# Optimization experiments

Hardware: AMD Instinct MI355X
Metric: run time of the kernel (lower is better)

The kernel has to match this reference:

```python
import jax, jax.numpy as jnp
import numpy as np

MOE_TOP_K = 2
MOE_GATE_NORM_STD = 1.0  # moe_gate_norm_std


def setup_inputs() -> dict:
    key = jax.random.key(0)
    k1, k2, k3, k4 = jax.random.split(key, 4)
    T, D, E = 16384, 2048, 8
    return {
        "x": jax.random.normal(k1, (T, D), dtype=jnp.float32),
        "wg_weight": jax.random.normal(k2, (E, D), dtype=jnp.float32) * 0.02,
        "gate_map_weight": jax.random.normal(k3, (E, E), dtype=jnp.float32) * 0.1,
        "gate_residual": jax.random.normal(k4, (T, E), dtype=jnp.float32),
    }


def reference(x, wg_weight, gate_map_weight, gate_residual):
    # Router GEMM in fp32 (module force-casts wg and input to float32)
    logits = jnp.einsum("td,ed->te", x.astype(jnp.float32), wg_weight)  # [T, E]
    # gate_residual path: gate_map Linear(E, E, bias=False)
    logits = logits + jnp.einsum("te,fe->tf", gate_residual, gate_map_weight)

    num_experts = wg_weight.shape[0]
    # gating(): moe_use_mixtral_gating=False, moe_use_logits_norm=True
    # torch.std is unbiased (ddof=1)
    logits_std = jnp.std(logits, axis=1, keepdims=True, ddof=1)
    probs = jax.nn.softmax(logits / (logits_std / MOE_GATE_NORM_STD), axis=1)
    gates, indices = jax.lax.top_k(probs, MOE_TOP_K)  # [T, K]
    # zero out routing to the last expert, then renormalize
    gates = jnp.where(indices == num_experts - 1, jnp.zeros_like(gates), gates)
    gates = gates / jnp.sum(gates, axis=1, keepdims=True)
    # Dense equivalent of the per-expert nonzero-gather dict: (indices, gates)
    # fully determines expert_info[e] = (tokens where indices==e, matching gates).
    return gates, indices, logits
```

## Files before the change

kernel.cpp:

```cpp
#include <hip/hip_runtime.h>
#include <hip/hip_bf16.h>
#include <stdint.h>


#define DCONST 2048

typedef float f32x4 __attribute__((ext_vector_type(4)));

__device__ __forceinline__ unsigned long long shfl_xor_u64(unsigned long long v, int m) {
    int lo = __shfl_xor((int)(uint32_t)v, m, 64);
    int hi = __shfl_xor((int)(uint32_t)(v >> 32), m, 64);
    return ((unsigned long long)(uint32_t)hi << 32) | (unsigned long long)(uint32_t)lo;
}

__global__ __launch_bounds__(256, 2)
void router_gemm(const float* __restrict__ x,
                 const float* __restrict__ wg,
                 float* __restrict__ ws,
                 int T)
{
    const int wave = threadIdx.x >> 6;
    const int lane = threadIdx.x & 63;
    const int W    = blockIdx.x * 4 + wave;

    #pragma unroll 1
    for (int s = 0; s < 2; ++s) {
        const int id    = W + s * 2048;
        const int g     = id & 7;
        const int trow  = (id >> 3) * 32;
        const int tb0   = trow >> 3;

        const float* wgp = wg + g * 256 + (lane << 2);
        f32x4 w8[8];
        #pragma unroll
        for (int e = 0; e < 8; ++e)
            w8[e] = *(const f32x4*)(wgp + (size_t)e * DCONST);

        const float* xp = x + (size_t)trow * DCONST + g * 256 + (lane << 2);

        f32x4 A[8], B[8];

        #define LOADB(buf, b)                                                 \
            { _Pragma("unroll")                                               \
              for (int i = 0; i < 8; ++i)                                     \
                  buf[i] = __builtin_nontemporal_load(                        \
                      (const f32x4*)(xp + (size_t)((b) * 8 + i) * DCONST)); }

        #define DOBATCH(buf, b)                                               \
            { float acc[64];                                                  \
              _Pragma("unroll")                                               \
              for (int v = 0; v < 64; ++v) acc[v] = 0.f;                      \
              _Pragma("unroll")                                               \
              for (int i = 0; i < 8; ++i) {                                   \
                  _Pragma("unroll")                                           \
                  for (int e = 0; e < 8; ++e) {                               \
                      float a = acc[i * 8 + e];                               \
                      a += buf[i].x * w8[e].x;                                \
                      a += buf[i].y * w8[e].y;                                \
                      a += buf[i].z * w8[e].z;                                \
                      a += buf[i].w * w8[e].w;                                \
                      acc[i * 8 + e] = a;                                     \
                  }                                                           \
              }                                                               \
              _Pragma("unroll")                                               \
              for (int m = 1; m < 64; m <<= 1) {                              \
                  const bool up = (lane & m) != 0;                            \
                  _Pragma("unroll")                                           \
                  for (int v = 0; v < 64; v += 2 * m) {                       \
                      const float keep = up ? acc[v + m] : acc[v];            \
                      const float send = up ? acc[v] : acc[v + m];            \
                      const float got  = __shfl_xor(send, m, 64);             \
                      acc[v] = keep + got;                                    \
                  }                                                           \
              }                                                               \
              ws[(size_t)(tb0 + (b)) * 512 + g * 64 + lane] = acc[0]; }

        LOADB(A, 0);
        #pragma unroll 1
        for (int b = 0; b < 4; b += 2) {
            LOADB(B, b + 1);
            DOBATCH(A, b);
            if (b + 2 < 4) LOADB(A, b + 2);
            DOBATCH(B, b + 1);
        }
    }
}

__global__ __launch_bounds__(256)
void router_epilogue(const float* __restrict__ ws,
                     const float* __restrict__ gm,
                     const float* __restrict__ gr,
                     float* __restrict__ out,
                     int T)
{
    const int wave = threadIdx.x >> 6;
    const int lane = threadIdx.x & 63;
    const int tb   = blockIdx.x * 4 + wave;
    const int t0   = tb * 8;

    float logit = 0.f;
    #pragma unroll
    for (int g = 0; g < 8; ++g)
        logit += ws[(size_t)tb * 512 + g * 64 + lane];

    const int tt = lane >> 3;
    const int f  = lane & 7;
    const int t  = t0 + tt;

    const float4 ga = *(const float4*)(gr + (size_t)t * 8);
    const float4 gb = *(const float4*)(gr + (size_t)t * 8 + 4);
    const float4 ma = *(const float4*)(gm + f * 8);
    const float4 mb = *(const float4*)(gm + f * 8 + 4);
    logit += ga.x * ma.x + ga.y * ma.y + ga.z * ma.z + ga.w * ma.w
           + gb.x * mb.x + gb.y * mb.y + gb.z * mb.z + gb.w * mb.w;

    out[(size_t)4 * T + (size_t)t0 * 8 + lane] = logit;

    float s = logit;
    s += __shfl_xor(s, 1, 64);
    s += __shfl_xor(s, 2, 64);
    s += __shfl_xor(s, 4, 64);
    const float mean = s * 0.125f;
    float d2 = (logit - mean) * (logit - mean);
    d2 += __shfl_xor(d2, 1, 64);
    d2 += __shfl_xor(d2, 2, 64);
    d2 += __shfl_xor(d2, 4, 64);
    const float stdv = sqrtf(d2 / 7.0f);

    uint32_t ob = __float_as_uint(logit);
    ob = (ob & 0x80000000u) ? ~ob : (ob | 0x80000000u);
    unsigned long long k1 = ((unsigned long long)ob << 8) | (unsigned long long)(7 - f);
    unsigned long long k2 = 0ull;
    #pragma unroll
    for (int m = 1; m <= 4; m <<= 1) {
        const unsigned long long o1 = shfl_xor_u64(k1, m);
        const unsigned long long o2 = shfl_xor_u64(k2, m);
        const unsigned long long hi = k1 > o1 ? k1 : o1;
        const unsigned long long lo = k1 > o1 ? o1 : k1;
        const unsigned long long so = k2 > o2 ? k2 : o2;
        k1 = hi;
        k2 = lo > so ? lo : so;
    }
    const int i1 = 7 - (int)(k1 & 0xFFull);
    const int i2 = 7 - (int)(k2 & 0xFFull);
    uint32_t b1 = (uint32_t)(k1 >> 8), b2 = (uint32_t)(k2 >> 8);
    b1 = (b1 & 0x80000000u) ? (b1 ^ 0x80000000u) : ~b1;
    b2 = (b2 & 0x80000000u) ? (b2 ^ 0x80000000u) : ~b2;
    const float l1 = __uint_as_float(b1);
    const float l2 = __uint_as_float(b2);

    float g0, g1;
    if (i1 == 7)      { g0 = 0.f; g1 = 1.f; }
    else if (i2 == 7) { g0 = 1.f; g1 = 0.f; }
    else {
        const float p = 1.0f / (1.0f + __expf(-(l1 - l2) / stdv));
        g0 = p; g1 = 1.0f - p;
    }

    if (f == 0) out[(size_t)2 * t]             = g0;
    if (f == 1) out[(size_t)2 * t + 1]         = g1;
    if (f == 2) out[(size_t)2 * T + 2 * t]     = (float)i1;
    if (f == 3) out[(size_t)2 * T + 2 * t + 1] = (float)i2;
}

extern "C" void kernel_launch(void* const* d_in, const int* in_sizes, int n_in,
                              void* d_out, int out_size, void* d_ws, size_t ws_size,
                              hipStream_t stream) {
    const float* x  = (const float*)d_in[0];
    const float* wg = (const float*)d_in[1];
    const float* gm = (const float*)d_in[2];
    const float* gr = (const float*)d_in[3];
    float* ws = (float*)d_ws;
    const int T = in_sizes[0] / DCONST;

    router_gemm<<<512, 256, 0, stream>>>(x, wg, ws, T);

    const int epi_blocks = T / 32;
    router_epilogue<<<epi_blocks, 256, 0, stream>>>(ws, gm, gr, (float*)d_out, T);
}
```

Measured before the change: 190.0 us.

## Stream router GEMM activations via direct global-to-LDS loads with double buffering

The activation tiles now go straight from global memory into per-wave LDS double buffers through global_load_lds, with hand-placed vmcnt waits. Previously they were loaded into registers with nontemporal loads. Each batch is read back from LDS into registers just before the FMA and shuffle reduction. The expert weight loads are also hoisted out of the two-pass loop, since the group index is the same on both passes. The aim is to free registers and overlap memory traffic with compute, at the cost of 64KB of LDS per block and fragile raw waitcnt encodings.

```diff
diff --git a/kernel.cpp b/kernel.cpp
--- a/kernel.cpp
+++ b/kernel.cpp
@@ -6,6 +6,12 @@
 #define DCONST 2048
 
 typedef float f32x4 __attribute__((ext_vector_type(4)));
+
+__device__ __forceinline__ void gload_lds16(const float* g, float* l) {
+    __builtin_amdgcn_global_load_lds(
+        (const __attribute__((address_space(1))) void*)g,
+        (__attribute__((address_space(3))) void*)l, 16, 0, 0);
+}
 
 __device__ __forceinline__ unsigned long long shfl_xor_u64(unsigned long long v, int m) {
     int lo = __shfl_xor((int)(uint32_t)v, m, 64);
@@ -23,31 +29,37 @@
     const int lane = threadIdx.x & 63;
     const int W    = blockIdx.x * 4 + wave;
 
+    __shared__ float lds[4][2][DCONST];
+    float* buf0 = &lds[wave][0][0];
+    float* buf1 = &lds[wave][1][0];
+
+    const int g     = W & 7;
+    const int trow0 = (W >> 3) * 32;
+
+    const float* wgp = wg + g * 256 + (lane << 2);
+    f32x4 w8[8];
+    #pragma unroll
+    for (int e = 0; e < 8; ++e)
+        w8[e] = *(const f32x4*)(wgp + (size_t)e * DCONST);
+
     #pragma unroll 1
     for (int s = 0; s < 2; ++s) {
-        const int id    = W + s * 2048;
-        const int g     = id & 7;
-        const int trow  = (id >> 3) * 32;
-        const int tb0   = trow >> 3;
-
-        const float* wgp = wg + g * 256 + (lane << 2);
-        f32x4 w8[8];
-        #pragma unroll
-        for (int e = 0; e < 8; ++e)
-            w8[e] = *(const f32x4*)(wgp + (size_t)e * DCONST);
-
+        const int trow = trow0 + s * 8192;
+        const int tb0  = trow >> 3;
         const float* xp = x + (size_t)trow * DCONST + g * 256 + (lane << 2);
 
-        f32x4 A[8], B[8];
-
-        #define LOADB(buf, b)                                                 \
+        #define LDSLOAD(dst, b)                                               \
             { _Pragma("unroll")                                               \
               for (int i = 0; i < 8; ++i)                                     \
-                  buf[i] = __builtin_nontemporal_load(                        \
-                      (const f32x4*)(xp + (size_t)((b) * 8 + i) * DCONST)); }
+                  gload_lds16(xp + (size_t)((b) * 8 + i) * DCONST,            \
+                              dst + i * 256); }
 
-        #define DOBATCH(buf, b)                                               \
-            { float acc[64];                                                  \
+        #define DOBATCH(src, b)                                               \
+            { f32x4 r[8];                                                     \
+              _Pragma("unroll")                                               \
+              for (int i = 0; i < 8; ++i)                                     \
+                  r[i] = *(const f32x4*)(src + i * 256 + (lane << 2));        \
+              float acc[64];                                                  \
               _Pragma("unroll")                                               \
               for (int v = 0; v < 64; ++v) acc[v] = 0.f;                      \
               _Pragma("unroll")                                               \
@@ -55,10 +67,10 @@
                   _Pragma("unroll")                                           \
                   for (int e = 0; e < 8; ++e) {                               \
                       float a = acc[i * 8 + e];                               \
-                      a += buf[i].x * w8[e].x;                                \
-                      a += buf[i].y * w8[e].y;                                \
-                      a += buf[i].z * w8[e].z;                                \
-                      a += buf[i].w * w8[e].w;                                \
+                      a += r[i].x * w8[e].x;                                  \
+                      a += r[i].y * w8[e].y;                                  \
+                      a += r[i].z * w8[e].z;                                  \
+                      a += r[i].w * w8[e].w;                                  \
                       acc[i * 8 + e] = a;                                     \
                   }                                                           \
               }                                                               \
@@ -75,14 +87,18 @@
               }                                                               \
               ws[(size_t)(tb0 + (b)) * 512 + g * 64 + lane] = acc[0]; }
 
-        LOADB(A, 0);
-        #pragma unroll 1
-        for (int b = 0; b < 4; b += 2) {
-            LOADB(B, b + 1);
-            DOBATCH(A, b);
-            if (b + 2 < 4) LOADB(A, b + 2);
-            DOBATCH(B, b + 1);
-        }
+        LDSLOAD(buf0, 0);
+        LDSLOAD(buf1, 1);
+        __builtin_amdgcn_s_waitcnt(0x0F78);
+        DOBATCH(buf0, 0);
+        LDSLOAD(buf0, 2);
+        __builtin_amdgcn_s_waitcnt(0x0F78);
+        DOBATCH(buf1, 1);
+        LDSLOAD(buf1, 3);
+        __builtin_amdgcn_s_waitcnt(0x0F78);
+        DOBATCH(buf0, 2);
+        __builtin_amdgcn_s_waitcnt(0x0F70);
+        DOBATCH(buf1, 3);
     }
 }
 
```

After: 199.4 us. 5.0% more time.
